# Kernel tuning notes

Measured on AMD Instinct MI355X. Metric: run time of the kernel, lower is better.

The kernel has to match this reference:

```python
import jax, jax.numpy as jnp
import numpy as np

B, H, W, C, M1, M2 = 16, 128, 128, 64, 16, 16
EPS = 1e-5


def setup_inputs() -> dict:
    key = jax.random.key(0)
    ks = jax.random.split(key, 9)
    scale = 1.0 / (C * C)  # torch FNO init: scale * rand(complex)
    inp = {
        "x": jax.random.normal(ks[0], (B * H * W, C), jnp.float32),
        "w1r": scale * jax.random.uniform(ks[1], (C, C, M1, M2), jnp.float32),
        "w1i": scale * jax.random.uniform(ks[2], (C, C, M1, M2), jnp.float32),
        "w2r": scale * jax.random.uniform(ks[3], (C, C, M1, M2), jnp.float32),
        "w2i": scale * jax.random.uniform(ks[4], (C, C, M1, M2), jnp.float32),
        "mlp_w1": 0.02 * jax.random.normal(ks[5], (2 * C, C), jnp.float32),
        "mlp_b1": 0.02 * jax.random.normal(ks[6], (2 * C,), jnp.float32),
        "mlp_w2": 0.02 * jax.random.normal(ks[7], (C, 2 * C), jnp.float32),
        "mlp_b2": 0.02 * jax.random.normal(ks[8], (C,), jnp.float32),
        "image_h": H,
        "image_w": W,
        "batch_size": B,
    }
    return inp


def instance_norm(x):
    # x: [b, c, h, w]; InstanceNorm2d(affine=False), biased variance, eps=1e-5
    mu = jnp.mean(x, axis=(2, 3), keepdims=True)
    var = jnp.var(x, axis=(2, 3), keepdims=True)
    return (x - mu) * jax.lax.rsqrt(var + EPS)


def spectral_conv(x, w1r, w1i, w2r, w2i, m1, m2):
    # x: [b, c, h, w] real
    b, c, h, w = x.shape
    x_ft = jnp.fft.rfft2(x, axes=(-2, -1))  # [b, c, h, w//2+1] complex
    w1 = w1r + 1j * w1i  # [ci, co, m1, m2]
    w2 = w2r + 1j * w2i
    top = jnp.einsum("bixy,ioxy->boxy", x_ft[:, :, :m1, :m2], w1)
    bot = jnp.einsum("bixy,ioxy->boxy", x_ft[:, :, -m1:, :m2], w2)
    out_ft = jnp.zeros((b, c, h, w // 2 + 1), dtype=x_ft.dtype)
    out_ft = out_ft.at[:, :, :m1, :m2].set(top)
    out_ft = out_ft.at[:, :, -m1:, :m2].set(bot)
    return jnp.fft.irfft2(out_ft, s=(h, w), axes=(-2, -1))


def conv_mlp(x, w1, b1, w2, b2):
    # two 1x1 convs with exact GELU between
    h = jnp.einsum("oc,bchw->bohw", w1, x) + b1[None, :, None, None]
    h = jax.nn.gelu(h, approximate=False)
    return jnp.einsum("oc,bchw->bohw", w2, h) + b2[None, :, None, None]


def reference(x, w1r, w1i, w2r, w2i, mlp_w1, mlp_b1, mlp_w2, mlp_b2,
              image_h, image_w, batch_size):
    c = x.shape[1]
    # (b h w) c -> b c h w
    x4 = x.reshape(batch_size, image_h, image_w, c).transpose(0, 3, 1, 2)
    y = instance_norm(spectral_conv(instance_norm(x4), w1r, w1i, w2r, w2i, M1, M2))
    y = conv_mlp(y, mlp_w1, mlp_b1, mlp_w2, mlp_b2)
    # b c h w -> (b h w) c
    return y.transpose(0, 2, 3, 1).reshape(batch_size * image_h * image_w, c)
```

## Files before the change

kernel.cpp:

```cpp
#include <hip/hip_runtime.h>
#include <hip/hip_bf16.h>
#include <math.h>

#define OFF_TBL 0u
#define OFF_S1  256u
#define OFF_S2  2304u
#define OFF_PQ  4352u
#define OFF_X   4198656u
#define OFF_O   5247232u
#define OFF_WT  6295808u

typedef __attribute__((ext_vector_type(8))) short bfrag;
typedef __attribute__((ext_vector_type(4))) float f4v;
#define MFMA(A,B,C) __builtin_amdgcn_mfma_f32_16x16x32_bf16(A,B,C,0,0,0)

#define F4GET(v, i) ((i)==0 ? (v).x : (i)==1 ? (v).y : (i)==2 ? (v).z : (v).w)

__device__ __forceinline__ unsigned short f2bf_rn(float x) {
    unsigned u = __float_as_uint(x);
    unsigned r = u + 0x7FFFu + ((u >> 16) & 1u);
    return (unsigned short)(r >> 16);
}
__device__ __forceinline__ unsigned short f2bf_n(float x) {
    __hip_bfloat16 b = __float2bfloat16(x);
    return __builtin_bit_cast(unsigned short, b);
}
__device__ __forceinline__ float bf2f(unsigned short h) {
    return __uint_as_float(((unsigned)h) << 16);
}
__device__ __forceinline__ void split2(float x, unsigned short& hi, unsigned short& lo) {
    hi = f2bf_rn(x);
    lo = f2bf_rn(x - bf2f(hi));
}
__device__ __forceinline__ float gelu_t(float x) {
    float t2 = x*x*x;
    float p = __builtin_fmaf(0.044715f, t2, x);
    float e = __expf(-1.5957691216057308f * p);
    return x * __builtin_amdgcn_rcpf(1.f + e);
}

__device__ __forceinline__ void gload_lds16(const float* g, float* l) {
    __builtin_amdgcn_global_load_lds(
        (const __attribute__((address_space(1))) void*)g,
        (__attribute__((address_space(3))) void*)l, 16, 0, 0);
}

__global__ void k_init(float* __restrict__ ws) {
    int t = threadIdx.x, bid = blockIdx.x;
    if (bid == 0) {
        if (t < 128) {
            double ang = 6.283185307179586476925286766559 * (double)t / 128.0;
            ws[OFF_TBL + 2*t]     = (float)cos(ang);
            ws[OFF_TBL + 2*t + 1] = (float)sin(ang);
        }
        for (int i = t; i < 4096; i += 256) ws[OFF_S1 + i] = 0.f;
        return;
    }
    int e = (bid - 1)*256 + t;
    unsigned short* OU = (unsigned short*)(ws + OFF_O);
    const double TWO_PI = 6.283185307179586476925286766559;
    if (e < 4096) {
        int row = e >> 7, w = e & 127, ky = row & 15;
        double ang = TWO_PI * (double)((ky * w) & 127) / 128.0;
        double v = (row < 16) ? cos(ang) : -sin(ang);
        unsigned short hi, lo; split2((float)v, hi, lo);
        OU[e] = hi; OU[4096 + e] = lo;
    } else {
        int e2 = e - 4096, row = e2 >> 7, h = e2 & 127;
        int kx = row >> 1, f = kx < 16 ? kx : 96 + kx;
        double ang = TWO_PI * (double)((f * h) & 127) / 128.0;
        double v = (row & 1) ? sin(ang) : cos(ang);
        unsigned short hi, lo; split2((float)v, hi, lo);
        OU[8192 + e2] = hi; OU[16384 + e2] = lo;
    }
}

__global__ __launch_bounds__(256) void k_big(const float* __restrict__ x,
        const float* __restrict__ w1r, const float* __restrict__ w1i,
        const float* __restrict__ w2r, const float* __restrict__ w2i,
        float* __restrict__ ws) {
    __shared__ __align__(16) char smem[33280];
    int bid = blockIdx.x;
    int t = threadIdx.x;
    if (bid < 512) {
        float* Xf = (float*)smem;
        int hp = bid & 31, b = bid >> 5;
        int l = t & 63, wv = t >> 6;
        const unsigned short* OU = (const unsigned short*)(ws + OFF_O);
        const unsigned short* FdAh = OU, *FdAl = OU + 4096;
        f4v acc[2][4];
        #pragma unroll
        for (int mt = 0; mt < 2; mt++)
            #pragma unroll
            for (int nt = 0; nt < 4; nt++) acc[mt][nt] = (f4v){0.f,0.f,0.f,0.f};
        float s1a[4] = {0,0,0,0}, s2a[4] = {0,0,0,0};
        const float* xb = x + ((long)(b*128 + hp*4 + wv))*8192;
        float* XfW = Xf + wv*2080;

        for (int kc = 0; kc < 4; kc++) {
            if (kc) {
                asm volatile("s_waitcnt lgkmcnt(0)" ::: "memory");
                __builtin_amdgcn_sched_barrier(0);
            }
            #pragma unroll
            for (int j = 0; j < 8; j++)
                gload_lds16(xb + (kc*32 + j*4)*64 + l*4, XfW + j*260);
            int kglob = kc*32 + (l >> 4)*8;
            bfrag mah[2], mal[2];
            #pragma unroll
            for (int mt = 0; mt < 2; mt++) {
                int row = mt*16 + (l & 15);
                mah[mt] = *(const bfrag*)(FdAh + row*128 + kglob);
                mal[mt] = *(const bfrag*)(FdAl + row*128 + kglob);
            }
            asm volatile("s_waitcnt vmcnt(0)" ::: "memory");
            __builtin_amdgcn_sched_barrier(0);
            #pragma unroll
            for (int nt = 0; nt < 4; nt++) {
                bfrag bh;
                #pragma unroll
                for (int j = 0; j < 8; j++) {
                    int k = (l >> 4)*8 + j;
                    float f = XfW[(k >> 2)*260 + (k & 3)*64 + nt*16 + (l & 15)];
                    s1a[nt] += f;
                    s2a[nt] += f*f;
                    bh[j] = (short)f2bf_rn(f);
                }
                #pragma unroll
                for (int mt = 0; mt < 2; mt++) {
                    f4v a_ = acc[mt][nt];
                    a_ = MFMA(mah[mt], bh, a_);
                    a_ = MFMA(mal[mt], bh, a_);
                    acc[mt][nt] = a_;
                }
            }
        }
        #pragma unroll
        for (int nt = 0; nt < 4; nt++) {
            s1a[nt] += __shfl_down(s1a[nt], 16, 64);
            s1a[nt] += __shfl_down(s1a[nt], 32, 64);
            s2a[nt] += __shfl_down(s2a[nt], 16, 64);
            s2a[nt] += __shfl_down(s2a[nt], 32, 64);
        }
        if (l < 16) {
            #pragma unroll
            for (int nt = 0; nt < 4; nt++) {
                int c = nt*16 + l;
                atomicAdd(&ws[OFF_S1 + (b*64 + c)*2],     s1a[nt]);
                atomicAdd(&ws[OFF_S1 + (b*64 + c)*2 + 1], s2a[nt]);
            }
        }
        __syncthreads();
        unsigned* TB = (unsigned*)smem;
        #pragma unroll
        for (int mt = 0; mt < 2; mt++)
            #pragma unroll
            for (int nt = 0; nt < 4; nt++)
                #pragma unroll
                for (int rr = 0; rr < 4; rr++) {
                    float v = acc[mt][nt][rr];
                    unsigned short hi, lo; split2(v, hi, lo);
                    int trow = mt*16 + (l >> 4)*4 + rr;
                    int ri = trow >> 4, ky = trow & 15;
                    int c = nt*16 + (l & 15);
                    TB[ky*520 + (c*2 + ri)*4 + wv] = ((unsigned)hi << 16) | lo;
                }
        __syncthreads();
        unsigned* PTb = (unsigned*)(ws + OFF_PQ) + ((long)(b*32 + hp))*8192;
        #pragma unroll
        for (int i = 0; i < 8; i++) {
            int idx = i*256 + t;
            int ky = idx >> 7, m = idx & 127;
            ((uint4*)PTb)[idx] = *(const uint4*)(TB + ky*520 + m*4);
        }
    } else {
        float* Lr = (float*)smem;
        float* Li = Lr + 16*257;
        int rel = bid - 512;
        int i = rel & 63, part = rel >> 6;
        float* WT = ws + OFF_WT;
        const float* wr = part ? w2r : w1r;
        const float* wi = part ? w2i : w1i;
        for (int oc = 0; oc < 4; oc++) {
            int o0 = oc * 16;
            __syncthreads();
            for (int idx = t; idx < 4096; idx += 256) {
                int oo = idx >> 8, m = idx & 255;
                Lr[oo*257 + m] = wr[(i*64 + o0 + oo)*256 + m];
                Li[oo*257 + m] = wi[(i*64 + o0 + oo)*256 + m];
            }
            __syncthreads();
            for (int idx = t; idx < 8192; idx += 256) {
                int mode = idx >> 5, rem = idx & 31, oo = rem >> 1, ri = rem & 1;
                float val = ri ? Li[oo*257 + mode] : Lr[oo*257 + mode];
                int gm = part*256 + mode;
                WT[((gm*64 + i)*64 + (o0 + oo))*2 + ri] = val;
            }
        }
    }
}

__global__ __launch_bounds__(256) void k_dfth(float* __restrict__ ws) {
    __shared__ unsigned Bsh[16384];
    int t = threadIdx.x;
    int ky = blockIdx.x, b = blockIdx.y;
    int l = t & 63, wv = t >> 6;
    char* bh_base = (char*)Bsh;
    char* bl_base = bh_base + 32768;
    const uint4* PT4 = (const uint4*)((const unsigned*)(ws + OFF_PQ));
    const unsigned short* OU = (const unsigned short*)(ws + OFF_O);
    const unsigned short* EdAh = OU + 8192, *EdAl = OU + 16384;

    #pragma unroll
    for (int i = 0; i < 16; i++) {
        int idx = i*256 + t;
        int hp = idx >> 7, n = idx & 127;
        uint4 v = PT4[((long)(b*32 + hp)*16 + ky)*128 + n];
        unsigned h01 = (v.x >> 16) | (v.y & 0xFFFF0000u);
        unsigned h23 = (v.z >> 16) | (v.w & 0xFFFF0000u);
        unsigned l01 = (v.x & 0xFFFFu) | (v.y << 16);
        unsigned l23 = (v.z & 0xFFFFu) | (v.w << 16);
        int kk = hp*4;
        unsigned ad = (unsigned)(n*256 + ((kk*2) ^ ((n & 7) << 4)));
        *(uint2*)(bh_base + ad) = make_uint2(h01, h23);
        *(uint2*)(bl_base + ad) = make_uint2(l01, l23);
    }
    bfrag ea_h[4], ea_l[4];
    #pragma unroll
    for (int kc = 0; kc < 4; kc++) {
        int off = (wv*16 + (l & 15))*128 + kc*32 + (l >> 4)*8;
        ea_h[kc] = *(const bfrag*)(EdAh + off);
        ea_l[kc] = *(const bfrag*)(EdAl + off);
    }
    __syncthreads();
    f4v acc[8];
    #pragma unroll
    for (int nt = 0; nt < 8; nt++) acc[nt] = (f4v){0.f,0.f,0.f,0.f};
    #pragma unroll
    for (int kc = 0; kc < 4; kc++)
        #pragma unroll
        for (int nt = 0; nt < 8; nt++) {
            int col = nt*16 + (l & 15);
            unsigned ro = (unsigned)(col*256 + ((kc*64 + (l >> 4)*16) ^ ((col & 7) << 4)));
            bfrag bh = *(const bfrag*)(bh_base + ro);
            bfrag bl = *(const bfrag*)(bl_base + ro);
            acc[nt] = MFMA(ea_h[kc], bh, acc[nt]);
            acc[nt] = MFMA(ea_h[kc], bl, acc[nt]);
            acc[nt] = MFMA(ea_l[kc], bh, acc[nt]);
        }
    float* X = ws + OFF_X;
    #pragma unroll
    for (int nt = 0; nt < 8; nt++)
        #pragma unroll
        for (int p = 0; p < 2; p++) {
            float s0 = acc[nt][2*p], s1 = acc[nt][2*p + 1];
            float partner = __shfl_xor(s1, 1, 64);
            float res = (l & 1) ? (s0 - partner) : (s0 + partner);
            int kx = wv*8 + (l >> 4)*2 + p;
            X[(((long)b*32 + kx)*16 + ky)*128 + nt*16 + (l & 15)] = res;
        }
}

__global__ void k_mix(float* __restrict__ ws) {
    __shared__ float Wsh[8192];
    __shared__ float Xs[2048];
    __shared__ float rhoT[1024];
    int t = threadIdx.x;
    int mode = blockIdx.x;
    int kxI = mode >> 4, ky = mode & 15;
    const float* WT = ws + OFF_WT;
    const float* X = ws + OFF_X;
    float* O = ws + OFF_O;
    for (int i = t; i < 1024; i += 256) {
        float a = ws[OFF_S1 + 2*i], s = ws[OFF_S1 + 2*i + 1];
        float m = a * (1.f/16384.f);
        float v = s * (1.f/16384.f) - m*m;
        rhoT[i] = rsqrtf(v + 1e-5f);
    }
    for (int idx = t; idx < 8192; idx += 256) Wsh[idx] = WT[(long)mode*8192 + idx];
    __syncthreads();
    for (int idx = t; idx < 2048; idx += 256) {
        int b = idx >> 7, r = idx & 127;
        Xs[idx] = X[((b*32 + kxI)*16 + ky)*128 + r] * rhoT[b*64 + (r >> 1)];
    }
    __syncthreads();
    int o = t & 63, bg = t >> 6;
    float accr[4] = {0,0,0,0}, acci[4] = {0,0,0,0};
    for (int i = 0; i < 64; i++) {
        float wr = Wsh[(i*64 + o)*2], wi = Wsh[(i*64 + o)*2 + 1];
        #pragma unroll
        for (int j = 0; j < 4; j++) {
            float xr = Xs[(bg*4 + j)*128 + 2*i], xi = Xs[(bg*4 + j)*128 + 2*i + 1];
            accr[j] += xr*wr - xi*wi;
            acci[j] += xr*wi + xi*wr;
        }
    }
    #pragma unroll
    for (int j = 0; j < 4; j++) {
        int b = bg*4 + j;
        float2* dst = (float2*)(O + ((b*32 + kxI)*16 + ky)*128);
        dst[o] = make_float2(accr[j], acci[j]);
    }
}

__global__ __launch_bounds__(256) void k_tail(const float* __restrict__ mw1,
        const float* __restrict__ mw2, float* __restrict__ ws) {
    __shared__ unsigned short BstH[128*70];
    __shared__ unsigned short BstL[128*70];
    __shared__ float tblL[256];
    __shared__ float redP[4][32][2];
    int bid = blockIdx.x, t = threadIdx.x;
    if (bid >= 256) {
        int i = (bid - 256)*256 + t;
        unsigned short* xu = (unsigned short*)(ws + OFF_X);
        if (i < 8192) {
            unsigned short hi, lo; split2(mw1[i], hi, lo);
            xu[i] = hi; xu[8192 + i] = lo;
        } else if (i < 16384) {
            int k = i - 8192;
            unsigned short hi, lo; split2(mw2[k], hi, lo);
            xu[16384 + k] = hi; xu[24576 + k] = lo;
        } else if (i < 20480) {
            int m = i - 16384;
            int w = m >> 5, k = m & 31;
            int ky = k >> 1;
            double ang = 6.283185307179586476925286766559 * (double)((ky * w) & 127) / 128.0;
            double v = (k & 1) ? -sin(ang) : cos(ang);
            double a = (ky == 0) ? 1.0 : 2.0;
            float val = (float)(v * a) * (1.f/16384.f);
            unsigned short hi, lo; split2(val, hi, lo);
            xu[32768 + m] = hi; xu[36864 + m] = lo;
        }
        return;
    }
    int ky = bid & 15, b = bid >> 4;
    int l = t & 63, wv = t >> 6;
    for (int i = t; i < 256; i += 256) tblL[i] = ws[OFF_TBL + i];
    const float4* O4 = (const float4*)(ws + OFF_O);

    float pw0 = 0.f, pw1 = 0.f;
    #pragma unroll
    for (int i = 0; i < 4; i++) {
        int idx = i*256 + t;
        int kx = idx >> 5, u = idx & 31;
        float4 v = O4[((long)(b*32 + kx)*16 + ky)*32 + u];
        pw0 += v.x*v.x + v.y*v.y;
        pw1 += v.z*v.z + v.w*v.w;
        int k0 = kx*2;
        #pragma unroll
        for (int p = 0; p < 2; p++) {
            float orr = p ? v.z : v.x;
            float oii = p ? v.w : v.y;
            int n0 = (u*2 + p)*2;
            int n1 = n0 + 1;
            unsigned short hi, lo;
            split2(orr, hi, lo);
            { unsigned ad = (unsigned)(n0*70 + (k0 ^ (8*(n0 & 7)))); BstH[ad]=hi; BstL[ad]=lo; }
            { unsigned ad = (unsigned)(n1*70 + ((k0+1) ^ (8*(n1 & 7)))); BstH[ad]=hi; BstL[ad]=lo; }
            split2(oii, hi, lo);
            { unsigned ad = (unsigned)(n1*70 + (k0 ^ (8*(n1 & 7)))); BstH[ad]=hi; BstL[ad]=lo; }
            split2(-oii, hi, lo);
            { unsigned ad = (unsigned)(n0*70 + ((k0+1) ^ (8*(n0 & 7)))); BstH[ad]=hi; BstL[ad]=lo; }
        }
    }
    pw0 += __shfl_down(pw0, 32, 64);
    pw1 += __shfl_down(pw1, 32, 64);
    if (l < 32) { redP[wv][l][0] = pw0; redP[wv][l][1] = pw1; }
    __syncthreads();
    if (t < 64) {
        int u = t >> 1, oo = t & 1;
        int o = t;
        float p = redP[0][u][oo] + redP[1][u][oo] + redP[2][u][oo] + redP[3][u][oo];
        float s2add = (ky == 0 ? 0.5f : 2.f) * p;
        if (ky == 0) {
            const float* Ob = ws + OFF_O + (long)b*65536;
            float ar0 = Ob[2*o], ai0 = Ob[2*o + 1];
            float t1 = ar0*ar0 - ai0*ai0;
            for (int k = 1; k <= 15; k++) {
                float xr = Ob[(k*16)*128 + 2*o],        xi = Ob[(k*16)*128 + 2*o + 1];
                float yr = Ob[((32-k)*16)*128 + 2*o],   yi = Ob[((32-k)*16)*128 + 2*o + 1];
                t1 += 2.f*(xr*yr - xi*yi);
            }
            s2add += 0.5f*t1;
            ws[OFF_S2 + (b*64 + o)*2] = ar0;
        }
        atomicAdd(&ws[OFF_S2 + (b*64 + o)*2 + 1], s2add * (1.f/16384.f));
    }
    bfrag ah_[2][2], al_[2][2];
    #pragma unroll
    for (int q = 0; q < 2; q++) {
        int h = (wv*2 + q)*16 + (l & 15);
        #pragma unroll
        for (int kcl = 0; kcl < 2; kcl++) {
            int kbase = kcl*32 + (l >> 4)*8;
            bfrag vh, vl;
            #pragma unroll
            for (int j = 0; j < 8; j++) {
                int k = kbase + j;
                int kx = k >> 1, f = kx < 16 ? kx : 96 + kx;
                int m = (f * h) & 127;
                float val = (k & 1) ? tblL[2*m + 1] : tblL[2*m];
                unsigned short hi, lo; split2(val, hi, lo);
                vh[j] = (short)hi; vl[j] = (short)lo;
            }
            ah_[q][kcl] = vh; al_[q][kcl] = vl;
        }
    }
    f4v acc[2][8];
    #pragma unroll
    for (int q = 0; q < 2; q++)
        #pragma unroll
        for (int nt = 0; nt < 8; nt++) acc[q][nt] = (f4v){0.f,0.f,0.f,0.f};
    #pragma unroll
    for (int kcl = 0; kcl < 2; kcl++)
        #pragma unroll
        for (int nt = 0; nt < 8; nt++) {
            int n = nt*16 + (l & 15);
            unsigned ku = (unsigned)((kcl*32 + (l >> 4)*8) ^ (8*(n & 7)));
            bfrag bh = *(const bfrag*)(BstH + n*70 + ku);
            bfrag bl = *(const bfrag*)(BstL + n*70 + ku);
            #pragma unroll
            for (int q = 0; q < 2; q++) {
                f4v a_ = acc[q][nt];
                a_ = MFMA(ah_[q][kcl], bh, a_);
                a_ = MFMA(ah_[q][kcl], bl, a_);
                a_ = MFMA(al_[q][kcl], bh, a_);
                acc[q][nt] = a_;
            }
        }
    float* Q = ws + OFF_PQ;
    #pragma unroll
    for (int q = 0; q < 2; q++)
        #pragma unroll
        for (int nt = 0; nt < 8; nt++)
            #pragma unroll
            for (int r = 0; r < 4; r++) {
                int h = (wv*2 + q)*16 + (l >> 4)*4 + r;
                Q[((long)(b*128 + h))*2048 + ky*128 + nt*16 + (l & 15)] = acc[q][nt][r];
            }
}

__global__ __launch_bounds__(256, 3) void k_mlp(const float* __restrict__ mb1,
                      const float* __restrict__ mb2,
                      float* __restrict__ out, const float* __restrict__ ws) {
    __shared__ unsigned short zhS[8192];
    __shared__ unsigned short w1hS[8192];
    __shared__ unsigned short w2hS[8192];
    __shared__ unsigned short qhS[2304];
    int t = threadIdx.x;
    int h = blockIdx.x, b = blockIdx.y;
    int l = t & 63, wv = t >> 6;

    const unsigned short* xu = (const unsigned short*)(ws + OFF_X);
    const unsigned short* w1hG = xu;
    const unsigned short* w2hG = xu + 16384;
    const unsigned short* MhG  = xu + 32768, *MlG  = xu + 36864;

    for (int ch = t; ch < 1024; ch += 256) {
        int j = ch >> 3, c0 = (ch & 7) * 8;
        unsigned off = (unsigned)(j*128 + c0*2) ^ (unsigned)((j & 7) << 4);
        *(bfrag*)((char*)w1hS + off) = *(const bfrag*)(w1hG + ch*8);
    }
    for (int ch = t; ch < 1024; ch += 256) {
        int o = ch >> 4, j0 = (ch & 15) * 8;
        unsigned off = (unsigned)(o*256 + j0*2) ^ (unsigned)((o & 15) << 4);
        *(bfrag*)((char*)w2hS + off) = *(const bfrag*)(w2hG + ch*8);
    }
    const float* Qp = ws + OFF_PQ + (long)(b*128 + h)*2048;
    for (int i = t; i < 2048; i += 256) {
        int c = i & 63, k = i >> 6;
        float v = Qp[(k >> 1)*128 + c*2 + (k & 1)];
        qhS[c*36 + k] = f2bf_n(v);
    }
    bfrag ma_h[2], ma_l[2];
    #pragma unroll
    for (int q = 0; q < 2; q++) {
        int w = (wv + 4*q)*16 + (l & 15);
        ma_h[q] = *(const bfrag*)(MhG + w*32 + (l >> 4)*8);
        ma_l[q] = *(const bfrag*)(MlG + w*32 + (l >> 4)*8);
    }
    float muA[4], rhA[4];
    #pragma unroll
    for (int ct = 0; ct < 4; ct++) {
        int c = ct*16 + (l & 15);
        float s1 = ws[OFF_S2 + (b*64 + c)*2], s2 = ws[OFF_S2 + (b*64 + c)*2 + 1];
        float m = s1 * (1.f/16384.f);
        float v = s2 * (1.f/16384.f) - m*m;
        muA[ct] = m; rhA[ct] = rsqrtf(v + 1e-5f);
    }
    __syncthreads();

    #pragma unroll
    for (int q = 0; q < 2; q++) {
        int wt = wv + 4*q;
        #pragma unroll
        for (int ct = 0; ct < 4; ct++) {
            unsigned ro = (unsigned)((ct*16 + (l & 15))*72 + (l >> 4)*16);
            bfrag bh = *(const bfrag*)((const char*)qhS + ro);
            f4v acc = {0.f, 0.f, 0.f, 0.f};
            acc = MFMA(ma_h[q], bh, acc);
            acc = MFMA(ma_l[q], bh, acc);
            float mu_ = muA[ct], rh_ = rhA[ct];
            int c = ct*16 + (l & 15);
            #pragma unroll
            for (int r = 0; r < 4; r++) {
                int w = wt*16 + (l >> 4)*4 + r;
                float z = (acc[r] - mu_) * rh_;
                unsigned off = (unsigned)(w*128 + c*2) ^ (unsigned)((w & 7) << 4);
                *(unsigned short*)((char*)zhS + off) = f2bf_n(z);
            }
        }
    }
    bfrag za[2][2];
    #pragma unroll
    for (int q = 0; q < 2; q++) {
        int w = (wv + 4*q)*16 + (l & 15);
        #pragma unroll
        for (int ks = 0; ks < 2; ks++) {
            unsigned off = (unsigned)(w*128 + (ks*32 + (l >> 4)*8)*2) ^ (unsigned)((w & 7) << 4);
            za[q][ks] = *(const bfrag*)((const char*)zhS + off);
        }
    }
    f4v accO[2][4];
    #pragma unroll
    for (int q = 0; q < 2; q++)
        #pragma unroll
        for (int ot = 0; ot < 4; ot++) accO[q][ot] = (f4v){0.f,0.f,0.f,0.f};

    unsigned short* hhS = zhS;
    #pragma unroll
    for (int jh = 0; jh < 2; jh++) {
        #pragma unroll
        for (int q = 0; q < 2; q++) {
            int wt = wv + 4*q;
            #pragma unroll
            for (int jt = 0; jt < 4; jt++) {
                int j = jh*64 + jt*16 + (l & 15);
                f4v acc = {0.f, 0.f, 0.f, 0.f};
                #pragma unroll
                for (int ks = 0; ks < 2; ks++) {
                    unsigned off = (unsigned)(j*128 + (ks*32 + (l >> 4)*8)*2) ^ (unsigned)((j & 7) << 4);
                    bfrag bh = *(const bfrag*)((const char*)w1hS + off);
                    acc = MFMA(za[q][ks], bh, acc);
                }
                float bj = mb1[j];
                #pragma unroll
                for (int r = 0; r < 4; r++) {
                    int w = wt*16 + (l >> 4)*4 + r;
                    float hv = gelu_t(acc[r] + bj);
                    int jl = jt*16 + (l & 15);
                    unsigned off = (unsigned)(w*128 + jl*2) ^ (unsigned)((w & 7) << 4);
                    *(unsigned short*)((char*)hhS + off) = f2bf_n(hv);
                }
            }
        }
        #pragma unroll
        for (int q = 0; q < 2; q++) {
            int w = (wv + 4*q)*16 + (l & 15);
            bfrag ha[2];
            #pragma unroll
            for (int ks = 0; ks < 2; ks++) {
                unsigned off = (unsigned)(w*128 + (ks*32 + (l >> 4)*8)*2) ^ (unsigned)((w & 7) << 4);
                ha[ks] = *(const bfrag*)((const char*)hhS + off);
            }
            #pragma unroll
            for (int ot = 0; ot < 4; ot++) {
                int o = ot*16 + (l & 15);
                f4v acc = accO[q][ot];
                #pragma unroll
                for (int ks = 0; ks < 2; ks++) {
                    int jj = jh*64 + ks*32 + (l >> 4)*8;
                    unsigned off = (unsigned)(o*256 + jj*2) ^ (unsigned)((o & 15) << 4);
                    bfrag bh = *(const bfrag*)((const char*)w2hS + off);
                    acc = MFMA(ha[ks], bh, acc);
                }
                accO[q][ot] = acc;
            }
        }
    }
    #pragma unroll
    for (int q = 0; q < 2; q++) {
        int wt = wv + 4*q;
        #pragma unroll
        for (int ot = 0; ot < 4; ot++) {
            int o = ot*16 + (l & 15);
            float bo = mb2[o];
            #pragma unroll
            for (int r = 0; r < 4; r++) {
                int w = wt*16 + (l >> 4)*4 + r;
                out[((long)(b*128 + h)*128 + w)*64 + o] = accO[q][ot][r] + bo;
            }
        }
    }
}

extern "C" void kernel_launch(void* const* d_in, const int* in_sizes, int n_in,
                              void* d_out, int out_size, void* d_ws, size_t ws_size,
                              hipStream_t stream) {
    const float* x   = (const float*)d_in[0];
    const float* w1r = (const float*)d_in[1];
    const float* w1i = (const float*)d_in[2];
    const float* w2r = (const float*)d_in[3];
    const float* w2i = (const float*)d_in[4];
    const float* mw1 = (const float*)d_in[5];
    const float* mb1 = (const float*)d_in[6];
    const float* mw2 = (const float*)d_in[7];
    const float* mb2 = (const float*)d_in[8];
    float* ws  = (float*)d_ws;
    float* out = (float*)d_out;

    k_init <<<dim3(49),      dim3(256), 0, stream>>>(ws);
    k_big  <<<dim3(640),     dim3(256), 0, stream>>>(x, w1r, w1i, w2r, w2i, ws);
    k_dfth <<<dim3(16,16),   dim3(256), 0, stream>>>(ws);
    k_mix  <<<dim3(512),     dim3(256), 0, stream>>>(ws);
    k_tail <<<dim3(336),     dim3(256), 0, stream>>>(mw1, mw2, ws);
    k_mlp  <<<dim3(128,16),  dim3(256), 0, stream>>>(mb1, mb2, out, ws);
}
```

Measured before the change: 97.58 us.

## Double-buffer x tile loads in the W-DFT stage to overlap with MFMA

Replaces the single per-wave LDS staging buffer in the first k_big phase with two buffers. The next k-chunk's global-to-LDS loads are issued before computing the current one, with vmcnt-based waits, and the DFT matrix fragments for all four chunks are preloaded into registers up front. This aims to hide global load latency behind the MFMA and statistics work. In exchange it doubles shared memory per block to 66560 bytes, which may cut occupancy, and adds register pressure.

```diff
diff --git a/kernel.cpp b/kernel.cpp
--- a/kernel.cpp
+++ b/kernel.cpp
@@ -79,7 +79,7 @@
         const float* __restrict__ w1r, const float* __restrict__ w1i,
         const float* __restrict__ w2r, const float* __restrict__ w2i,
         float* __restrict__ ws) {
-    __shared__ __align__(16) char smem[33280];
+    __shared__ __align__(16) char smem[66560];
     int bid = blockIdx.x;
     int t = threadIdx.x;
     if (bid < 512) {
@@ -95,46 +95,68 @@
             for (int nt = 0; nt < 4; nt++) acc[mt][nt] = (f4v){0.f,0.f,0.f,0.f};
         float s1a[4] = {0,0,0,0}, s2a[4] = {0,0,0,0};
         const float* xb = x + ((long)(b*128 + hp*4 + wv))*8192;
-        float* XfW = Xf + wv*2080;
-
+        float* buf0 = Xf + wv*4160;
+        float* buf1 = buf0 + 2080;
+
+        bfrag mah[4][2], mal[4][2];
+        #pragma unroll
         for (int kc = 0; kc < 4; kc++) {
-            if (kc) {
-                asm volatile("s_waitcnt lgkmcnt(0)" ::: "memory");
-                __builtin_amdgcn_sched_barrier(0);
-            }
-            #pragma unroll
-            for (int j = 0; j < 8; j++)
-                gload_lds16(xb + (kc*32 + j*4)*64 + l*4, XfW + j*260);
             int kglob = kc*32 + (l >> 4)*8;
-            bfrag mah[2], mal[2];
             #pragma unroll
             for (int mt = 0; mt < 2; mt++) {
                 int row = mt*16 + (l & 15);
-                mah[mt] = *(const bfrag*)(FdAh + row*128 + kglob);
-                mal[mt] = *(const bfrag*)(FdAl + row*128 + kglob);
-            }
-            asm volatile("s_waitcnt vmcnt(0)" ::: "memory");
-            __builtin_amdgcn_sched_barrier(0);
-            #pragma unroll
-            for (int nt = 0; nt < 4; nt++) {
-                bfrag bh;
-                #pragma unroll
-                for (int j = 0; j < 8; j++) {
-                    int k = (l >> 4)*8 + j;
-                    float f = XfW[(k >> 2)*260 + (k & 3)*64 + nt*16 + (l & 15)];
-                    s1a[nt] += f;
-                    s2a[nt] += f*f;
-                    bh[j] = (short)f2bf_rn(f);
-                }
-                #pragma unroll
-                for (int mt = 0; mt < 2; mt++) {
-                    f4v a_ = acc[mt][nt];
-                    a_ = MFMA(mah[mt], bh, a_);
-                    a_ = MFMA(mal[mt], bh, a_);
-                    acc[mt][nt] = a_;
-                }
-            }
-        }
+                mah[kc][mt] = *(const bfrag*)(FdAh + row*128 + kglob);
+                mal[kc][mt] = *(const bfrag*)(FdAl + row*128 + kglob);
+            }
+        }
+        #define DFTW_ISSUE(KC, BUF)                                           \
+            _Pragma("unroll")                                                 \
+            for (int j = 0; j < 8; j++)                                       \
+                gload_lds16(xb + ((KC)*32 + j*4)*64 + l*4, (BUF) + j*260);
+        #define DFTW_COMPUTE(KC, BUF)                                         \
+            _Pragma("unroll")                                                 \
+            for (int nt = 0; nt < 4; nt++) {                                  \
+                bfrag bh;                                                     \
+                _Pragma("unroll")                                             \
+                for (int j = 0; j < 8; j++) {                                 \
+                    int k = (l >> 4)*8 + j;                                   \
+                    float f = (BUF)[(k >> 2)*260 + (k & 3)*64 + nt*16 + (l & 15)]; \
+                    s1a[nt] += f;                                             \
+                    s2a[nt] += f*f;                                           \
+                    bh[j] = (short)f2bf_rn(f);                                \
+                }                                                             \
+                _Pragma("unroll")                                             \
+                for (int mt = 0; mt < 2; mt++) {                              \
+                    f4v a_ = acc[mt][nt];                                     \
+                    a_ = MFMA(mah[KC][mt], bh, a_);                           \
+                    a_ = MFMA(mal[KC][mt], bh, a_);                           \
+                    acc[mt][nt] = a_;                                         \
+                }                                                             \
+            }
+
+        DFTW_ISSUE(0, buf0);
+        DFTW_ISSUE(1, buf1);
+        asm volatile("s_waitcnt vmcnt(8)" ::: "memory");
+        __builtin_amdgcn_sched_barrier(0);
+        DFTW_COMPUTE(0, buf0);
+        asm volatile("s_waitcnt lgkmcnt(0)" ::: "memory");
+        __builtin_amdgcn_sched_barrier(0);
+        DFTW_ISSUE(2, buf0);
+        asm volatile("s_waitcnt vmcnt(8)" ::: "memory");
+        __builtin_amdgcn_sched_barrier(0);
+        DFTW_COMPUTE(1, buf1);
+        asm volatile("s_waitcnt lgkmcnt(0)" ::: "memory");
+        __builtin_amdgcn_sched_barrier(0);
+        DFTW_ISSUE(3, buf1);
+        asm volatile("s_waitcnt vmcnt(8)" ::: "memory");
+        __builtin_amdgcn_sched_barrier(0);
+        DFTW_COMPUTE(2, buf0);
+        asm volatile("s_waitcnt vmcnt(0)" ::: "memory");
+        __builtin_amdgcn_sched_barrier(0);
+        DFTW_COMPUTE(3, buf1);
+        #undef DFTW_ISSUE
+        #undef DFTW_COMPUTE
+
         #pragma unroll
         for (int nt = 0; nt < 4; nt++) {
             s1a[nt] += __shfl_down(s1a[nt], 16, 64);
```

Result: slower. 100.1 us (+2.5%).
